# Kernel tuning notes

Hardware: AMD Instinct MI355X
Metric: run time of the kernel (lower is better)

## Reference

```python
import jax, jax.numpy as jnp
import numpy as np

NEG_SLOPE_GAT = 0.2   # PyG GATConv default negative_slope
NEG_SLOPE = 0.01      # torch.nn.LeakyReLU default
NUM_AISLES = 20       # aisle_nrs drawn from [0,20); matches aisle_nrs.max()+1


def leaky(x, s):
    return jnp.where(x >= 0, x, s * x)


def gat_conv(x, src, dst, W, a_src, a_dst, b, n_nodes):
    """Single-head PyG GATConv (self-loops already appended to src/dst)."""
    h = x @ W                                        # [N, C]
    es = h @ a_src                                   # [N]
    ed = h @ a_dst                                   # [N]
    e = leaky(es[src] + ed[dst], NEG_SLOPE_GAT)      # [E] per-edge score
    m = jax.ops.segment_max(e, dst, num_segments=n_nodes)
    w = jnp.exp(e - m[dst])
    z = jax.ops.segment_sum(w, dst, num_segments=n_nodes)
    alpha = w / z[dst]                               # segment softmax over incoming edges
    out = jax.ops.segment_sum(h[src] * alpha[:, None], dst, num_segments=n_nodes)
    return out + b


def setup_inputs() -> dict:
    key = jax.random.key(0)
    ks = jax.random.split(key, 32)
    B, N, E = 16, 2048, 32768
    Fin, H, O, HA = 32, 128, 64, 256

    def glorot(k, shape):
        fan = shape[0] + shape[-1]
        return jax.random.uniform(k, shape, jnp.float32, -1.0, 1.0) * np.sqrt(6.0 / fan)

    inp = {
        "graph_nodes": jax.random.normal(ks[0], (B, N, Fin), jnp.float32),
        "aisle_nrs": jax.random.randint(ks[1], (B, N), 0, NUM_AISLES),
        "graph_edge_links": jax.random.randint(ks[2], (B, 2, E), 0, N),
        "mask": jax.random.randint(ks[3], (B, N), 0, 2),
        "picks_left": jax.random.randint(ks[4], (B,), 0, 100),
        # GAT layer 1: Fin -> H
        "W1": glorot(ks[5], (Fin, H)), "as1": glorot(ks[6], (H,)), "ad1": glorot(ks[7], (H,)), "b1": jnp.zeros((H,), jnp.float32),
        # GAT layer 2: H -> H
        "W2": glorot(ks[8], (H, H)), "as2": glorot(ks[9], (H,)), "ad2": glorot(ks[10], (H,)), "b2": jnp.zeros((H,), jnp.float32),
        # GAT layer 3: H -> O
        "W3": glorot(ks[11], (H, O)), "as3": glorot(ks[12], (O,)), "ad3": glorot(ks[13], (O,)), "b3": jnp.zeros((O,), jnp.float32),
        # post-embedding MLP head
        "lw1": glorot(ks[14], (2 * O, HA)), "lb1": jnp.zeros((HA,), jnp.float32),
        "lw2": glorot(ks[15], (HA, O)), "lb2": jnp.zeros((O,), jnp.float32),
        "lw3": glorot(ks[16], (O, 1)), "lb3": jnp.zeros((1,), jnp.float32),
    }
    return inp


def reference(graph_nodes, aisle_nrs, graph_edge_links, mask, picks_left,
              W1, as1, ad1, b1, W2, as2, ad2, b2, W3, as3, ad3, b3,
              lw1, lb1, lw2, lb2, lw3, lb3):
    B, N, Fin = graph_nodes.shape
    NT = B * N
    x = graph_nodes.reshape(NT, Fin)

    # batch the graphs: offset per-graph edge indices, append self-loops
    off = (jnp.arange(B) * N)[:, None]
    src = (graph_edge_links[:, 0, :] + off).reshape(-1)
    dst = (graph_edge_links[:, 1, :] + off).reshape(-1)
    loops = jnp.arange(NT)
    src = jnp.concatenate([src, loops])
    dst = jnp.concatenate([dst, loops])

    x = gat_conv(x, src, dst, W1, as1, ad1, b1, NT)
    x = gat_conv(x, src, dst, W2, as2, ad2, b2, NT)
    x = gat_conv(x, src, dst, W3, as3, ad3, b3, NT)

    # scatter-mean aisle embedding
    batch_idx = jnp.repeat(jnp.arange(B), N)
    aid = aisle_nrs.reshape(-1) + batch_idx * NUM_AISLES   # [NT]
    S = B * NUM_AISLES
    ssum = jax.ops.segment_sum(x, aid, num_segments=S)
    cnt = jax.ops.segment_sum(jnp.ones((NT,), x.dtype), aid, num_segments=S)
    emb = ssum / jnp.maximum(cnt, 1.0)[:, None]

    x = jnp.concatenate([x, emb[aid]], axis=1)             # [NT, 2*O]
    x = leaky(x @ lw1 + lb1, NEG_SLOPE)
    x = leaky(x @ lw2 + lb2, NEG_SLOPE)
    x = (x @ lw3 + lb3).reshape(B, N)

    logits = jnp.where(mask != 0, x, -jnp.inf)
    return jax.nn.softmax(logits, axis=1)
```

## Files before the change

kernel.cpp:

```cpp
#include <hip/hip_runtime.h>
#include <hip/hip_bf16.h>
#include <math.h>
#include <stdint.h>

#define BATCH 16
#define NNODE 2048
#define EPG   32768
#define NT    (BATCH * NNODE)
#define ET    (BATCH * EPG + NT)
#define NUM_AISLES 20
#define SEG   (BATCH * NUM_AISLES)
#define NEG_GAT 0.2f
#define NEG_MLP 0.01f
#define ACHUNK 8
#define CAP 64
#define EMB_LD 72

typedef __attribute__((ext_vector_type(8))) short s16x8;
typedef __attribute__((ext_vector_type(4))) float f32x4;

__device__ __forceinline__ void split_bf16(float v, unsigned short& hi, unsigned short& lo) {
    unsigned int u = __float_as_uint(v);
    unsigned int r = u + 0x7FFFu + ((u >> 16) & 1u);
    hi = (unsigned short)(r >> 16);
    float fh = __uint_as_float(((unsigned int)hi) << 16);
    float rem = v - fh;
    unsigned int u2 = __float_as_uint(rem);
    unsigned int r2 = u2 + 0x7FFFu + ((u2 >> 16) & 1u);
    lo = (unsigned short)(r2 >> 16);
}

__device__ __forceinline__ unsigned int pack_bf16(float v) {
    unsigned short h, l;
    split_bf16(v, h, l);
    return ((unsigned int)h << 16) | l;
}

__device__ __forceinline__ float unpack_f32(unsigned int u) {
    return __uint_as_float(u & 0xffff0000u) + __uint_as_float(u << 16);
}

__device__ __forceinline__ int swz_row0(int bx) {
    int xcd = bx & 7, i = bx >> 3;
    int graph = xcd * 2 + (i >> 5);
    return graph * NNODE + (i & 31) * 64;
}

template <int K, int KC, int NOUT, int COLS>
__device__ __forceinline__ void prep_one(const float* __restrict__ W,
                                         unsigned short* __restrict__ dst, int idx) {
    constexpr int SWM = (KC >= 64) ? 7 : 3;
    int k = idx / NOUT, col = idx - k * NOUT;
    int ch = k / KC, kl = k - ch * KC;
    int ct = col / COLS, n = col - ct * COLS;
    int tile = ct * (K / KC) + ch;
    unsigned short h, l;
    split_bf16(W[idx], h, l);
    size_t base = (size_t)tile * (2 * COLS * KC);
    int pos = n * KC + (kl ^ ((n & SWM) << 3));
    dst[base + pos] = h;
    dst[base + COLS * KC + pos] = l;
}

__global__ __launch_bounds__(256) void prep_weights(const float* __restrict__ W1,
                                                    const float* __restrict__ W2,
                                                    const float* __restrict__ W3,
                                                    const float* __restrict__ lw1,
                                                    const float* __restrict__ lw2,
                                                    unsigned short* __restrict__ P1,
                                                    unsigned short* __restrict__ P2,
                                                    unsigned short* __restrict__ P3,
                                                    unsigned short* __restrict__ P4,
                                                    unsigned short* __restrict__ P5,
                                                    int* __restrict__ cnt) {
    int b = blockIdx.x, t = threadIdx.x;
    if (b < 16)        prep_one<32, 32, 128, 128>(W1, P1, b * 256 + t);
    else if (b < 80)   prep_one<128, 64, 128, 128>(W2, P2, (b - 16) * 256 + t);
    else if (b < 112)  prep_one<128, 128, 64, 64>(W3, P3, (b - 80) * 256 + t);
    else if (b < 240)  prep_one<128, 64, 256, 128>(lw1, P4, (b - 112) * 256 + t);
    else if (b < 304)  prep_one<256, 128, 64, 64>(lw2, P5, (b - 240) * 256 + t);
    else               cnt[(b - 304) * 256 + t] = 0;
}

__device__ __forceinline__ void scatter_body(int b, const int* __restrict__ links,
                                             int* __restrict__ cnt,
                                             int* __restrict__ col_bkt) {
    int s, d;
    if (b < 2048) {
        int xcd = b & 7, idx = b >> 3;
        int g = xcd * 2 + (idx >> 7);
        int chunk = idx & 127;
        int i = chunk * 256 + threadIdx.x;
        const int* pb = links + (size_t)g * 2 * EPG;
        s = pb[i] + (g << 11);
        d = pb[EPG + i] + (g << 11);
    } else {
        int b2 = b - 2048;
        int xcd = b2 & 7, idx = b2 >> 3;
        int g = xcd * 2 + (idx >> 3);
        int chunk = idx & 7;
        s = d = g * NNODE + chunk * 256 + threadIdx.x;
    }
    int pos = atomicAdd(&cnt[d], 1);
    if (pos < CAP) col_bkt[d * CAP + pos] = s;
}

template <int K, int KC, int NOUT, int COLS, bool LEAKY, bool ATTN, bool FINAL,
          bool CONCAT, bool PACKEDA, bool PACKOUT>
__device__ __forceinline__ void gemm_body(int bx, int by,
                                          const void* __restrict__ Aptr,
                                          const unsigned short* __restrict__ WP,
                                          const float* __restrict__ bias,
                                          void* __restrict__ outp,
                                          const float* __restrict__ a_src,
                                          const float* __restrict__ a_dst,
                                          float* __restrict__ es,
                                          float* __restrict__ ed,
                                          const float* __restrict__ psum,
                                          const int* __restrict__ pcnt,
                                          const int* __restrict__ aisle,
                                          const float* __restrict__ lw3,
                                          const float* __restrict__ lb3,
                                          const int* __restrict__ mask,
                                          float* __restrict__ logits) {
    constexpr int C = COLS / 16;
    constexpr int SWM = (KC >= 64) ? 7 : 3;
    constexpr int TILE_US = COLS * KC;
    constexpr int TB2 = 2 * TILE_US * 2;
    static_assert(TB2 % 4096 == 0, "chunk must be a multiple of one 256-thread 16B sweep");

    __shared__ unsigned short WS[2 * TILE_US];
    __shared__ float emb_s[CONCAT ? NUM_AISLES * EMB_LD : 1];

    const int tid = threadIdx.x;
    const int wave = tid >> 6, lane = tid & 63;
    const int quad = lane >> 4, l15 = lane & 15;
    const int row0 = swz_row0(bx);
    const int m = row0 + wave * 16 + l15;

    int am = 0;
    if constexpr (CONCAT) {
        int g = row0 >> 11;
        for (int i = tid; i < NUM_AISLES * 64; i += 256) {
            int a = i >> 6, f = i & 63;
            float s = 0.f;
            int c = 0;
#pragma unroll
            for (int ch = 0; ch < ACHUNK; ++ch) {
                s += psum[((size_t)(g * ACHUNK + ch) * NUM_AISLES + a) * 64 + f];
                c += pcnt[(g * ACHUNK + ch) * NUM_AISLES + a];
            }
            emb_s[a * EMB_LD + f] = s / fmaxf((float)c, 1.0f);
        }
        am = aisle[m];
    }

    f32x4 acc[C];
#pragma unroll
    for (int c = 0; c < C; ++c)
#pragma unroll
        for (int v = 0; v < 4; ++v) acc[c][v] = 0.f;

    union SU { s16x8 v; unsigned short u[8]; };

    for (int kb = 0; kb < K; kb += KC) {
        const char* gsrc = (const char*)WP
            + (size_t)(by * (K / KC) + kb / KC) * TB2;
#pragma unroll
        for (int s = 0; s < TB2 / 4096; ++s) {
            __builtin_amdgcn_global_load_lds(
                (const __attribute__((address_space(1))) void*)(gsrc + s * 4096 + wave * 1024 + lane * 16),
                (__attribute__((address_space(3))) void*)&WS[(s * 4096 + wave * 1024) >> 1],
                16, 0, 0);
        }
        __syncthreads();

        for (int kc = kb; kc < kb + KC; kc += 32) {
            const int off = kc + quad * 8;
            SU ah, al;
            if constexpr (CONCAT) {
                if (off < 64) {
                    const unsigned int* ap = (const unsigned int*)Aptr + (size_t)m * 64 + off;
                    uint4 u0 = ((const uint4*)ap)[0];
                    uint4 u1 = ((const uint4*)ap)[1];
                    unsigned int uu[8] = {u0.x, u0.y, u0.z, u0.w, u1.x, u1.y, u1.z, u1.w};
#pragma unroll
                    for (int j = 0; j < 8; ++j) {
                        ah.u[j] = (unsigned short)(uu[j] >> 16);
                        al.u[j] = (unsigned short)uu[j];
                    }
                } else {
                    const float* ep = &emb_s[am * EMB_LD + (off - 64)];
                    float4 v0 = ((const float4*)ep)[0];
                    float4 v1 = ((const float4*)ep)[1];
                    float a8[8] = {v0.x, v0.y, v0.z, v0.w, v1.x, v1.y, v1.z, v1.w};
#pragma unroll
                    for (int j = 0; j < 8; ++j) split_bf16(a8[j], ah.u[j], al.u[j]);
                }
            } else if constexpr (PACKEDA) {
                const unsigned int* ap = (const unsigned int*)Aptr + (size_t)m * K + off;
                uint4 u0 = ((const uint4*)ap)[0];
                uint4 u1 = ((const uint4*)ap)[1];
                unsigned int uu[8] = {u0.x, u0.y, u0.z, u0.w, u1.x, u1.y, u1.z, u1.w};
#pragma unroll
                for (int j = 0; j < 8; ++j) {
                    ah.u[j] = (unsigned short)(uu[j] >> 16);
                    al.u[j] = (unsigned short)uu[j];
                }
            } else {
                const float* srcp = (const float*)Aptr + (size_t)m * K + off;
                float4 v0 = ((const float4*)srcp)[0];
                float4 v1 = ((const float4*)srcp)[1];
                float a8[8] = {v0.x, v0.y, v0.z, v0.w, v1.x, v1.y, v1.z, v1.w};
#pragma unroll
                for (int j = 0; j < 8; ++j) split_bf16(a8[j], ah.u[j], al.u[j]);
            }

            const int kq = (kc - kb) + quad * 8;
#pragma unroll
            for (int c = 0; c < C; ++c) {
                int n = c * 16 + l15;
                int pos = n * KC + (kq ^ ((n & SWM) << 3));
                s16x8 wh = *(const s16x8*)&WS[pos];
                s16x8 wl = *(const s16x8*)&WS[TILE_US + pos];
                acc[c] = __builtin_amdgcn_mfma_f32_16x16x32_bf16(ah.v, wh, acc[c], 0, 0, 0);
                acc[c] = __builtin_amdgcn_mfma_f32_16x16x32_bf16(ah.v, wl, acc[c], 0, 0, 0);
                acc[c] = __builtin_amdgcn_mfma_f32_16x16x32_bf16(al.v, wh, acc[c], 0, 0, 0);
            }
        }
        if (kb + KC < K) __syncthreads();
    }
    if constexpr (FINAL) {
#pragma unroll
        for (int reg = 0; reg < 4; ++reg) {
            float p = 0.f;
#pragma unroll
            for (int c = 0; c < C; ++c) {
                int colx = c * 16 + l15;
                float v = acc[c][reg] + bias[colx];
                v = v >= 0.f ? v : NEG_MLP * v;
                p += v * lw3[colx];
            }
#pragma unroll
            for (int mk = 1; mk < 16; mk <<= 1) p += __shfl_xor(p, mk, 64);
            if (l15 == 0) {
                int row = row0 + wave * 16 + quad * 4 + reg;
                float lg = p + lb3[0];
                logits[row] = (mask[row] != 0) ? lg : -INFINITY;
            }
        }
    } else {
#pragma unroll
        for (int c = 0; c < C; ++c) {
            int colx = by * COLS + c * 16 + l15;
            float bv = bias ? bias[colx] : 0.f;
#pragma unroll
            for (int reg = 0; reg < 4; ++reg) {
                int row = row0 + wave * 16 + quad * 4 + reg;
                float v = acc[c][reg] + bv;
                if (LEAKY) v = v >= 0.f ? v : NEG_MLP * v;
                if constexpr (PACKOUT) {
                    ((unsigned int*)outp)[(size_t)row * NOUT + colx] = pack_bf16(v);
                } else {
                    ((float*)outp)[(size_t)row * NOUT + colx] = v;
                }
            }
        }
        if constexpr (ATTN) {
#pragma unroll
            for (int reg = 0; reg < 4; ++reg) {
                float ps = 0.f, pd = 0.f;
#pragma unroll
                for (int c = 0; c < C; ++c) {
                    int colx = c * 16 + l15;
                    float v = acc[c][reg];
                    ps += v * a_src[colx];
                    pd += v * a_dst[colx];
                }
#pragma unroll
                for (int mk = 1; mk < 16; mk <<= 1) {
                    ps += __shfl_xor(ps, mk, 64);
                    pd += __shfl_xor(pd, mk, 64);
                }
                if (l15 == 0) {
                    int row = row0 + wave * 16 + quad * 4 + reg;
                    es[row] = ps;
                    ed[row] = pd;
                }
            }
        }
    }
}

template <int K, int KC, int NOUT, int COLS, bool LEAKY, bool ATTN, bool FINAL,
          bool CONCAT, bool PACKEDA, bool PACKOUT>
__global__ __launch_bounds__(256) void gemm_mfma(const void* __restrict__ A,
                                                 const unsigned short* __restrict__ WP,
                                                 const float* __restrict__ bias,
                                                 void* __restrict__ out,
                                                 const float* __restrict__ a_src,
                                                 const float* __restrict__ a_dst,
                                                 float* __restrict__ es,
                                                 float* __restrict__ ed,
                                                 const float* __restrict__ psum,
                                                 const int* __restrict__ pcnt,
                                                 const int* __restrict__ aisle,
                                                 const float* __restrict__ lw3,
                                                 const float* __restrict__ lb3,
                                                 const int* __restrict__ mask,
                                                 float* __restrict__ logits) {
    gemm_body<K, KC, NOUT, COLS, LEAKY, ATTN, FINAL, CONCAT, PACKEDA, PACKOUT>(
        blockIdx.x, blockIdx.y, A, WP, bias, out, a_src, a_dst, es, ed,
        psum, pcnt, aisle, lw3, lb3, mask, logits);
}

__global__ __launch_bounds__(256) void gemm1_scatter(const float* __restrict__ A,
                                                     const unsigned short* __restrict__ WP,
                                                     float* __restrict__ out,
                                                     const float* __restrict__ a_src,
                                                     const float* __restrict__ a_dst,
                                                     float* __restrict__ es,
                                                     float* __restrict__ ed,
                                                     const int* __restrict__ links,
                                                     int* __restrict__ cnt,
                                                     int* __restrict__ col_bkt) {
    if (blockIdx.x >= NT / 64) {
        scatter_body(blockIdx.x - NT / 64, links, cnt, col_bkt);
        return;
    }
    gemm_body<32, 32, 128, 128, false, true, false, false, false, false>(
        blockIdx.x, 0, A, WP, nullptr, out, a_src, a_dst, es, ed,
        nullptr, nullptr, nullptr, nullptr, nullptr, nullptr, nullptr);
}

template <int HD>
__global__ __launch_bounds__(256) void gat_aggregate(const float* __restrict__ h,
                                                     const float* __restrict__ es,
                                                     const float* __restrict__ ed,
                                                     const int* __restrict__ cnt,
                                                     const int* __restrict__ col_bkt,
                                                     const float* __restrict__ bias,
                                                     unsigned int* __restrict__ out) {
    int b = blockIdx.x;
    int xcd = b & 7, q = b >> 3;
    int graph = xcd * 2 + (q >> 9);
    int node = graph * NNODE + (q & 511) * 4 + (threadIdx.x >> 6);
    int lane = threadIdx.x & 63;
    int deg = cnt[node];
    deg = deg < CAP ? deg : CAP;
    float edv = ed[node];

    float e0 = -INFINITY;
    int c0v = 0;
    if (lane < deg) {
        c0v = col_bkt[node * CAP + lane];
        float e = es[c0v] + edv;
        e0 = e >= 0.f ? e : NEG_GAT * e;
    }
    float m = e0;
#pragma unroll
    for (int off = 32; off; off >>= 1) m = fmaxf(m, __shfl_xor(m, off, 64));
    float z = __expf(e0 - m);
#pragma unroll
    for (int off = 32; off; off >>= 1) z += __shfl_xor(z, off, 64);
    float w0 = __expf(e0 - m) / z;

    const int quad = lane >> 4, l15 = lane & 15;
    if (HD == 128) {
        float a0 = 0.f, a1 = 0.f, a2 = 0.f, a3 = 0.f;
        float a4 = 0.f, a5 = 0.f, a6 = 0.f, a7 = 0.f;
        for (int jj = 0; jj < deg; jj += 4) {
            int j2 = jj + quad;
            int s = __shfl(c0v, j2, 64);
            float w = __shfl(w0, j2, 64);
            const float* base = h + (size_t)s * 128 + l15 * 8;
            float4 v0 = *(const float4*)base;
            float4 v1 = *(const float4*)(base + 4);
            a0 += w * v0.x; a1 += w * v0.y; a2 += w * v0.z; a3 += w * v0.w;
            a4 += w * v1.x; a5 += w * v1.y; a6 += w * v1.z; a7 += w * v1.w;
        }
#pragma unroll
        for (int off = 16; off <= 32; off <<= 1) {
            a0 += __shfl_xor(a0, off, 64); a1 += __shfl_xor(a1, off, 64);
            a2 += __shfl_xor(a2, off, 64); a3 += __shfl_xor(a3, off, 64);
            a4 += __shfl_xor(a4, off, 64); a5 += __shfl_xor(a5, off, 64);
            a6 += __shfl_xor(a6, off, 64); a7 += __shfl_xor(a7, off, 64);
        }
        if (quad == 0) {
            const float* bb = bias + l15 * 8;
            uint4 p0, p1;
            p0.x = pack_bf16(a0 + bb[0]); p0.y = pack_bf16(a1 + bb[1]);
            p0.z = pack_bf16(a2 + bb[2]); p0.w = pack_bf16(a3 + bb[3]);
            p1.x = pack_bf16(a4 + bb[4]); p1.y = pack_bf16(a5 + bb[5]);
            p1.z = pack_bf16(a6 + bb[6]); p1.w = pack_bf16(a7 + bb[7]);
            unsigned int* op = out + (size_t)node * 128 + l15 * 8;
            *(uint4*)op = p0;
            *(uint4*)(op + 4) = p1;
        }
    } else {
        float a0 = 0.f, a1 = 0.f, a2 = 0.f, a3 = 0.f;
        for (int jj = 0; jj < deg; jj += 4) {
            int j2 = jj + quad;
            int s = __shfl(c0v, j2, 64);
            float w = __shfl(w0, j2, 64);
            float4 v = *(const float4*)(h + (size_t)s * 64 + l15 * 4);
            a0 += w * v.x; a1 += w * v.y; a2 += w * v.z; a3 += w * v.w;
        }
#pragma unroll
        for (int off = 16; off <= 32; off <<= 1) {
            a0 += __shfl_xor(a0, off, 64); a1 += __shfl_xor(a1, off, 64);
            a2 += __shfl_xor(a2, off, 64); a3 += __shfl_xor(a3, off, 64);
        }
        if (quad == 0) {
            const float* bb = bias + l15 * 4;
            uint4 p;
            p.x = pack_bf16(a0 + bb[0]); p.y = pack_bf16(a1 + bb[1]);
            p.z = pack_bf16(a2 + bb[2]); p.w = pack_bf16(a3 + bb[3]);
            *(uint4*)(out + (size_t)node * 64 + l15 * 4) = p;
        }
    }
}

__global__ __launch_bounds__(256) void aisle_partial(const unsigned int* __restrict__ x3,
                                                     const int* __restrict__ aisle,
                                                     float* __restrict__ psum,
                                                     int* __restrict__ pcnt) {
    int xcd = blockIdx.x & 7, idx = blockIdx.x >> 3;
    int g = xcd * 2 + (idx >> 3);
    int ch = idx & 7;
    int pb = g * ACHUNK + ch;
    int f = threadIdx.x & 63;
    int stripe = threadIdx.x >> 6;

    __shared__ float sacc[4][NUM_AISLES][64];
    __shared__ int scnt[4][NUM_AISLES];
    for (int i = threadIdx.x; i < 4 * NUM_AISLES * 64; i += 256)
        ((float*)sacc)[i] = 0.f;
    for (int i = threadIdx.x; i < 4 * NUM_AISLES; i += 256)
        ((int*)scnt)[i] = 0;
    __syncthreads();

    const int* ai = aisle + g * NNODE;
    const unsigned int* xg = x3 + (size_t)g * NNODE * 64;
    int n0 = ch * 256 + stripe * 64;
#pragma unroll 4
    for (int i = 0; i < 64; ++i) {
        int n = n0 + i;
        int a = ai[n];
        float v = unpack_f32(xg[(size_t)n * 64 + f]);
        sacc[stripe][a][f] += v;
        if (f == 0) scnt[stripe][a]++;
    }
    __syncthreads();

    for (int i = threadIdx.x; i < NUM_AISLES * 64; i += 256) {
        int a = i >> 6, ff = i & 63;
        psum[((size_t)pb * NUM_AISLES + a) * 64 + ff] =
            sacc[0][a][ff] + sacc[1][a][ff] + sacc[2][a][ff] + sacc[3][a][ff];
    }
    for (int i = threadIdx.x; i < NUM_AISLES; i += 256) {
        pcnt[pb * NUM_AISLES + i] =
            scnt[0][i] + scnt[1][i] + scnt[2][i] + scnt[3][i];
    }
}

__global__ __launch_bounds__(256) void softmax_kernel(const float* __restrict__ logits,
                                                      float* __restrict__ out) {
    int b = blockIdx.x;
    const float* lr = logits + b * NNODE;
    __shared__ float red[4], redz[4];
    float m = -INFINITY;
    for (int i = threadIdx.x; i < NNODE; i += 256) m = fmaxf(m, lr[i]);
#pragma unroll
    for (int off = 32; off; off >>= 1) m = fmaxf(m, __shfl_xor(m, off, 64));
    if ((threadIdx.x & 63) == 0) red[threadIdx.x >> 6] = m;
    __syncthreads();
    m = fmaxf(fmaxf(red[0], red[1]), fmaxf(red[2], red[3]));
    float z = 0.f;
    for (int i = threadIdx.x; i < NNODE; i += 256) z += __expf(lr[i] - m);
#pragma unroll
    for (int off = 32; off; off >>= 1) z += __shfl_xor(z, off, 64);
    if ((threadIdx.x & 63) == 0) redz[threadIdx.x >> 6] = z;
    __syncthreads();
    z = redz[0] + redz[1] + redz[2] + redz[3];
    float invz = 1.0f / z;
    for (int i = threadIdx.x; i < NNODE; i += 256) {
        float v = lr[i];
        out[b * NNODE + i] = (v == -INFINITY) ? 0.f : __expf(v - m) * invz;
    }
}


extern "C" void kernel_launch(void* const* d_in, const int* in_sizes, int n_in,
                              void* d_out, int out_size, void* d_ws, size_t ws_size,
                              hipStream_t stream) {
    const float* gn   = (const float*)d_in[0];
    const int* aisle  = (const int*)d_in[1];
    const int* links  = (const int*)d_in[2];
    const int* mask   = (const int*)d_in[3];
    const float* W1  = (const float*)d_in[5];
    const float* as1 = (const float*)d_in[6];
    const float* ad1 = (const float*)d_in[7];
    const float* b1  = (const float*)d_in[8];
    const float* W2  = (const float*)d_in[9];
    const float* as2 = (const float*)d_in[10];
    const float* ad2 = (const float*)d_in[11];
    const float* b2  = (const float*)d_in[12];
    const float* W3  = (const float*)d_in[13];
    const float* as3 = (const float*)d_in[14];
    const float* ad3 = (const float*)d_in[15];
    const float* b3  = (const float*)d_in[16];
    const float* lw1 = (const float*)d_in[17];
    const float* lb1 = (const float*)d_in[18];
    const float* lw2 = (const float*)d_in[19];
    const float* lb2 = (const float*)d_in[20];
    const float* lw3 = (const float*)d_in[21];
    const float* lb3 = (const float*)d_in[22];
    float* out = (float*)d_out;

    float* ws = (float*)d_ws;
    float* h      = ws;
    float* xb     = h + (size_t)NT * 128;
    float* es     = xb + (size_t)NT * 128;
    float* ed     = es + NT;
    float* emb    = ed + NT;
    float* y1     = emb + SEG * 64;
    float* y2     = y1 + (size_t)NT * 256;
    float* logits = y2 + (size_t)NT * 64;
    float* psum   = logits + NT;
    int* pcnt     = (int*)(psum + 128 * NUM_AISLES * 64);
    int* row_ptr  = pcnt + 128 * NUM_AISLES;
    int* cnt      = row_ptr + NT + 1;
    int* col_bkt  = (int*)y2;

    unsigned short* wsplit = (unsigned short*)(((uintptr_t)(cnt + NT) + 255) & ~(uintptr_t)255);
    unsigned short* P1 = wsplit;
    unsigned short* P2 = P1 + 8192;
    unsigned short* P3 = P2 + 32768;
    unsigned short* P4 = P3 + 16384;
    unsigned short* P5 = P4 + 65536;

    const int EB = (ET + 255) / 256;

    prep_weights<<<432, 256, 0, stream>>>(W1, W2, W3, lw1, lw2, P1, P2, P3, P4, P5, cnt);

    gemm1_scatter<<<NT / 64 + EB, 256, 0, stream>>>(gn, P1, h, as1, ad1, es, ed,
                                                    links, cnt, col_bkt);
    gat_aggregate<128><<<NT / 4, 256, 0, stream>>>(h, es, ed, cnt, col_bkt, b1, (unsigned int*)xb);

    gemm_mfma<128, 64, 128, 128, false, true, false, false, true, false><<<dim3(NT / 64, 1), 256, 0, stream>>>(
        xb, P2, nullptr, h, as2, ad2, es, ed, nullptr, nullptr, nullptr, nullptr, nullptr, nullptr, nullptr);
    gat_aggregate<128><<<NT / 4, 256, 0, stream>>>(h, es, ed, cnt, col_bkt, b2, (unsigned int*)xb);

    gemm_mfma<128, 128, 64, 64, false, true, false, false, true, false><<<dim3(NT / 64, 1), 256, 0, stream>>>(
        xb, P3, nullptr, h, as3, ad3, es, ed, nullptr, nullptr, nullptr, nullptr, nullptr, nullptr, nullptr);
    gat_aggregate<64><<<NT / 4, 256, 0, stream>>>(h, es, ed, cnt, col_bkt, b3, (unsigned int*)xb);

    aisle_partial<<<BATCH * ACHUNK, 256, 0, stream>>>((const unsigned int*)xb, aisle, psum, pcnt);

    gemm_mfma<128, 64, 256, 128, true, false, false, true, false, true><<<dim3(NT / 64, 2), 256, 0, stream>>>(
        xb, P4, lb1, y1, nullptr, nullptr, nullptr, nullptr, psum, pcnt, aisle, nullptr, nullptr, nullptr, nullptr);

    gemm_mfma<256, 128, 64, 64, true, false, true, false, true, false><<<dim3(NT / 64, 1), 256, 0, stream>>>(
        y1, P5, lb2, nullptr, nullptr, nullptr, nullptr, nullptr, nullptr, nullptr, nullptr, lw3, lb3, mask, logits);

    softmax_kernel<<<BATCH, 256, 0, stream>>>(logits, out);
}
```

Measured before the change: 279.1 us.

## Fuse all stages into one cooperative persistent kernel with grid syncs

Replaces the sequence of about ten kernel launches (weight prep, GEMM plus edge scatter, three aggregations, aisle partials, MLP GEMMs, softmax) with one cooperative persistent kernel. Each stage loops over virtual block indices and a grid-wide sync separates stages. Static shared buffers become a single shared arena that the stage bodies carve up. This aims to remove launch gaps and tail effects between stages. The cost is grid-sync overhead, a grid capped at 1024 blocks, the loss of the per-stage XCD-aware block mapping in some stages, and occupancy limited by the union of the stages' register and shared-memory needs.

Result: slower. 935.9 us (+235.3%).

```diff
diff --git a/kernel.cpp b/kernel.cpp
--- a/kernel.cpp
+++ b/kernel.cpp
@@ -1,7 +1,10 @@
 #include <hip/hip_runtime.h>
+#include <hip/hip_cooperative_groups.h>
 #include <hip/hip_bf16.h>
 #include <math.h>
 #include <stdint.h>
+
+namespace cg = cooperative_groups;
 
 #define BATCH 16
 #define NNODE 2048
@@ -15,6 +18,7 @@
 #define ACHUNK 8
 #define CAP 64
 #define EMB_LD 72
+#define SMEM_BYTES 38528
 
 typedef __attribute__((ext_vector_type(8))) short s16x8;
 typedef __attribute__((ext_vector_type(4))) float f32x4;
@@ -62,18 +66,19 @@
     dst[base + COLS * KC + pos] = l;
 }
 
-__global__ __launch_bounds__(256) void prep_weights(const float* __restrict__ W1,
-                                                    const float* __restrict__ W2,
-                                                    const float* __restrict__ W3,
-                                                    const float* __restrict__ lw1,
-                                                    const float* __restrict__ lw2,
-                                                    unsigned short* __restrict__ P1,
-                                                    unsigned short* __restrict__ P2,
-                                                    unsigned short* __restrict__ P3,
-                                                    unsigned short* __restrict__ P4,
-                                                    unsigned short* __restrict__ P5,
-                                                    int* __restrict__ cnt) {
-    int b = blockIdx.x, t = threadIdx.x;
+__device__ __forceinline__ void prep_body(int b,
+                                          const float* __restrict__ W1,
+                                          const float* __restrict__ W2,
+                                          const float* __restrict__ W3,
+                                          const float* __restrict__ lw1,
+                                          const float* __restrict__ lw2,
+                                          unsigned short* __restrict__ P1,
+                                          unsigned short* __restrict__ P2,
+                                          unsigned short* __restrict__ P3,
+                                          unsigned short* __restrict__ P4,
+                                          unsigned short* __restrict__ P5,
+                                          int* __restrict__ cnt) {
+    int t = threadIdx.x;
     if (b < 16)        prep_one<32, 32, 128, 128>(W1, P1, b * 256 + t);
     else if (b < 80)   prep_one<128, 64, 128, 128>(W2, P2, (b - 16) * 256 + t);
     else if (b < 112)  prep_one<128, 128, 64, 64>(W3, P3, (b - 80) * 256 + t);
@@ -107,7 +112,7 @@
 
 template <int K, int KC, int NOUT, int COLS, bool LEAKY, bool ATTN, bool FINAL,
           bool CONCAT, bool PACKEDA, bool PACKOUT>
-__device__ __forceinline__ void gemm_body(int bx, int by,
+__device__ __forceinline__ void gemm_body(int bx, int by, unsigned char* smem,
                                           const void* __restrict__ Aptr,
                                           const unsigned short* __restrict__ WP,
                                           const float* __restrict__ bias,
@@ -128,9 +133,12 @@
     constexpr int TILE_US = COLS * KC;
     constexpr int TB2 = 2 * TILE_US * 2;
     static_assert(TB2 % 4096 == 0, "chunk must be a multiple of one 256-thread 16B sweep");
-
-    __shared__ unsigned short WS[2 * TILE_US];
-    __shared__ float emb_s[CONCAT ? NUM_AISLES * EMB_LD : 1];
+    static_assert(TB2 <= 32768, "W-stage arena overflow");
+
+    unsigned short* WS = (unsigned short*)smem;
+    float* emb_s = (float*)(smem + 32768);
+
+    __syncthreads();
 
     const int tid = threadIdx.x;
     const int wave = tid >> 6, lane = tid & 63;
@@ -292,56 +300,15 @@
     }
 }
 
-template <int K, int KC, int NOUT, int COLS, bool LEAKY, bool ATTN, bool FINAL,
-          bool CONCAT, bool PACKEDA, bool PACKOUT>
-__global__ __launch_bounds__(256) void gemm_mfma(const void* __restrict__ A,
-                                                 const unsigned short* __restrict__ WP,
-                                                 const float* __restrict__ bias,
-                                                 void* __restrict__ out,
-                                                 const float* __restrict__ a_src,
-                                                 const float* __restrict__ a_dst,
-                                                 float* __restrict__ es,
-                                                 float* __restrict__ ed,
-                                                 const float* __restrict__ psum,
-                                                 const int* __restrict__ pcnt,
-                                                 const int* __restrict__ aisle,
-                                                 const float* __restrict__ lw3,
-                                                 const float* __restrict__ lb3,
-                                                 const int* __restrict__ mask,
-                                                 float* __restrict__ logits) {
-    gemm_body<K, KC, NOUT, COLS, LEAKY, ATTN, FINAL, CONCAT, PACKEDA, PACKOUT>(
-        blockIdx.x, blockIdx.y, A, WP, bias, out, a_src, a_dst, es, ed,
-        psum, pcnt, aisle, lw3, lb3, mask, logits);
-}
-
-__global__ __launch_bounds__(256) void gemm1_scatter(const float* __restrict__ A,
-                                                     const unsigned short* __restrict__ WP,
-                                                     float* __restrict__ out,
-                                                     const float* __restrict__ a_src,
-                                                     const float* __restrict__ a_dst,
-                                                     float* __restrict__ es,
-                                                     float* __restrict__ ed,
-                                                     const int* __restrict__ links,
-                                                     int* __restrict__ cnt,
-                                                     int* __restrict__ col_bkt) {
-    if (blockIdx.x >= NT / 64) {
-        scatter_body(blockIdx.x - NT / 64, links, cnt, col_bkt);
-        return;
-    }
-    gemm_body<32, 32, 128, 128, false, true, false, false, false, false>(
-        blockIdx.x, 0, A, WP, nullptr, out, a_src, a_dst, es, ed,
-        nullptr, nullptr, nullptr, nullptr, nullptr, nullptr, nullptr);
-}
-
 template <int HD>
-__global__ __launch_bounds__(256) void gat_aggregate(const float* __restrict__ h,
-                                                     const float* __restrict__ es,
-                                                     const float* __restrict__ ed,
-                                                     const int* __restrict__ cnt,
-                                                     const int* __restrict__ col_bkt,
-                                                     const float* __restrict__ bias,
-                                                     unsigned int* __restrict__ out) {
-    int b = blockIdx.x;
+__device__ __forceinline__ void agg_body(int b,
+                                         const float* __restrict__ h,
+                                         const float* __restrict__ es,
+                                         const float* __restrict__ ed,
+                                         const int* __restrict__ cnt,
+                                         const int* __restrict__ col_bkt,
+                                         const float* __restrict__ bias,
+                                         unsigned int* __restrict__ out) {
     int xcd = b & 7, q = b >> 3;
     int graph = xcd * 2 + (q >> 9);
     int node = graph * NNODE + (q & 511) * 4 + (threadIdx.x >> 6);
@@ -421,23 +388,22 @@
     }
 }
 
-__global__ __launch_bounds__(256) void aisle_partial(const unsigned int* __restrict__ x3,
-                                                     const int* __restrict__ aisle,
-                                                     float* __restrict__ psum,
-                                                     int* __restrict__ pcnt) {
-    int xcd = blockIdx.x & 7, idx = blockIdx.x >> 3;
-    int g = xcd * 2 + (idx >> 3);
-    int ch = idx & 7;
-    int pb = g * ACHUNK + ch;
+__device__ __forceinline__ void partial_body(int b, unsigned char* smem,
+                                             const unsigned int* __restrict__ x3,
+                                             const int* __restrict__ aisle,
+                                             float* __restrict__ psum,
+                                             int* __restrict__ pcnt) {
+    int g = b >> 3;
+    int ch = b & 7;
     int f = threadIdx.x & 63;
     int stripe = threadIdx.x >> 6;
 
-    __shared__ float sacc[4][NUM_AISLES][64];
-    __shared__ int scnt[4][NUM_AISLES];
-    for (int i = threadIdx.x; i < 4 * NUM_AISLES * 64; i += 256)
-        ((float*)sacc)[i] = 0.f;
-    for (int i = threadIdx.x; i < 4 * NUM_AISLES; i += 256)
-        ((int*)scnt)[i] = 0;
+    float* sacc = (float*)smem;
+    int* scnt = (int*)(smem + 20480);
+
+    __syncthreads();
+    for (int i = threadIdx.x; i < 4 * NUM_AISLES * 64; i += 256) sacc[i] = 0.f;
+    for (int i = threadIdx.x; i < 4 * NUM_AISLES; i += 256) scnt[i] = 0;
     __syncthreads();
 
     const int* ai = aisle + g * NNODE;
@@ -448,27 +414,31 @@
         int n = n0 + i;
         int a = ai[n];
         float v = unpack_f32(xg[(size_t)n * 64 + f]);
-        sacc[stripe][a][f] += v;
-        if (f == 0) scnt[stripe][a]++;
+        sacc[(stripe * NUM_AISLES + a) * 64 + f] += v;
+        if (f == 0) scnt[stripe * NUM_AISLES + a]++;
     }
     __syncthreads();
 
     for (int i = threadIdx.x; i < NUM_AISLES * 64; i += 256) {
         int a = i >> 6, ff = i & 63;
-        psum[((size_t)pb * NUM_AISLES + a) * 64 + ff] =
-            sacc[0][a][ff] + sacc[1][a][ff] + sacc[2][a][ff] + sacc[3][a][ff];
+        psum[((size_t)b * NUM_AISLES + a) * 64 + ff] =
+            sacc[(0 * NUM_AISLES + a) * 64 + ff] + sacc[(1 * NUM_AISLES + a) * 64 + ff] +
+            sacc[(2 * NUM_AISLES + a) * 64 + ff] + sacc[(3 * NUM_AISLES + a) * 64 + ff];
     }
     for (int i = threadIdx.x; i < NUM_AISLES; i += 256) {
-        pcnt[pb * NUM_AISLES + i] =
-            scnt[0][i] + scnt[1][i] + scnt[2][i] + scnt[3][i];
-    }
-}
-
-__global__ __launch_bounds__(256) void softmax_kernel(const float* __restrict__ logits,
-                                                      float* __restrict__ out) {
-    int b = blockIdx.x;
+        pcnt[b * NUM_AISLES + i] =
+            scnt[0 * NUM_AISLES + i] + scnt[1 * NUM_AISLES + i] +
+            scnt[2 * NUM_AISLES + i] + scnt[3 * NUM_AISLES + i];
+    }
+}
+
+__device__ __forceinline__ void softmax_body(int b, unsigned char* smem,
+                                             const float* __restrict__ logits,
+                                             float* __restrict__ out) {
     const float* lr = logits + b * NNODE;
-    __shared__ float red[4], redz[4];
+    float* red = (float*)smem;
+    float* redz = red + 4;
+    __syncthreads();
     float m = -INFINITY;
     for (int i = threadIdx.x; i < NNODE; i += 256) m = fmaxf(m, lr[i]);
 #pragma unroll
@@ -488,6 +458,94 @@
         float v = lr[i];
         out[b * NNODE + i] = (v == -INFINITY) ? 0.f : __expf(v - m) * invz;
     }
+}
+
+__global__ __launch_bounds__(256, 4) void mega(
+    const float* __restrict__ gn, const int* __restrict__ aisle,
+    const int* __restrict__ links, const int* __restrict__ mask,
+    const float* __restrict__ W1, const float* __restrict__ as1,
+    const float* __restrict__ ad1, const float* __restrict__ b1,
+    const float* __restrict__ W2, const float* __restrict__ as2,
+    const float* __restrict__ ad2, const float* __restrict__ b2,
+    const float* __restrict__ W3, const float* __restrict__ as3,
+    const float* __restrict__ ad3, const float* __restrict__ b3,
+    const float* __restrict__ lw1, const float* __restrict__ lb1,
+    const float* __restrict__ lw2, const float* __restrict__ lb2,
+    const float* __restrict__ lw3, const float* __restrict__ lb3,
+    float* __restrict__ h, unsigned int* __restrict__ xb,
+    float* __restrict__ es, float* __restrict__ ed,
+    unsigned int* __restrict__ y1, float* __restrict__ logits,
+    float* __restrict__ psum, int* __restrict__ pcnt,
+    int* __restrict__ cnt, int* __restrict__ col_bkt,
+    unsigned short* __restrict__ P1, unsigned short* __restrict__ P2,
+    unsigned short* __restrict__ P3, unsigned short* __restrict__ P4,
+    unsigned short* __restrict__ P5, float* __restrict__ out) {
+    cg::grid_group grid = cg::this_grid();
+    const int b0 = blockIdx.x;
+    const int nb = gridDim.x;
+    __shared__ alignas(16) unsigned char smem[SMEM_BYTES];
+
+    for (int vb = b0; vb < 432; vb += nb)
+        prep_body(vb, W1, W2, W3, lw1, lw2, P1, P2, P3, P4, P5, cnt);
+    grid.sync();
+
+    for (int vb = b0; vb < 2688; vb += nb) {
+        if (vb < 512)
+            gemm_body<32, 32, 128, 128, false, true, false, false, false, false>(
+                vb, 0, smem, gn, P1, nullptr, (void*)h, as1, ad1, es, ed,
+                nullptr, nullptr, nullptr, nullptr, nullptr, nullptr, nullptr);
+        else
+            scatter_body(vb - 512, links, cnt, col_bkt);
+    }
+    grid.sync();
+
+    for (int vb = b0; vb < 8192; vb += nb)
+        agg_body<128>(vb, h, es, ed, cnt, col_bkt, b1, xb);
+    grid.sync();
+
+    for (int vb = b0; vb < 1024; vb += nb)
+        if ((vb & 1) == 0)
+            gemm_body<128, 64, 128, 128, false, true, false, false, true, false>(
+                vb >> 1, 0, smem, xb, P2, nullptr, (void*)h, as2, ad2, es, ed,
+                nullptr, nullptr, nullptr, nullptr, nullptr, nullptr, nullptr);
+    grid.sync();
+
+    for (int vb = b0; vb < 8192; vb += nb)
+        agg_body<128>(vb, h, es, ed, cnt, col_bkt, b2, xb);
+    grid.sync();
+
+    for (int vb = b0; vb < 1024; vb += nb)
+        if ((vb & 1) == 0)
+            gemm_body<128, 128, 64, 64, false, true, false, false, true, false>(
+                vb >> 1, 0, smem, xb, P3, nullptr, (void*)h, as3, ad3, es, ed,
+                nullptr, nullptr, nullptr, nullptr, nullptr, nullptr, nullptr);
+    grid.sync();
+
+    for (int vb = b0; vb < 8192; vb += nb)
+        agg_body<64>(vb, h, es, ed, cnt, col_bkt, b3, xb);
+    grid.sync();
+
+    for (int vb = b0; vb < 1024; vb += nb)
+        if ((vb & 7) == 0)
+            partial_body(vb >> 3, smem, xb, aisle, psum, pcnt);
+    grid.sync();
+
+    for (int vb = b0; vb < 1024; vb += nb)
+        gemm_body<128, 64, 256, 128, true, false, false, true, false, true>(
+            vb & 511, vb >> 9, smem, xb, P4, lb1, (void*)y1, nullptr, nullptr,
+            nullptr, nullptr, psum, pcnt, aisle, nullptr, nullptr, nullptr, nullptr);
+    grid.sync();
+
+    for (int vb = b0; vb < 1024; vb += nb)
+        if ((vb & 1) == 0)
+            gemm_body<256, 128, 64, 64, true, false, true, false, true, false>(
+                vb >> 1, 0, smem, y1, P5, lb2, nullptr, nullptr, nullptr,
+                nullptr, nullptr, nullptr, nullptr, nullptr, lw3, lb3, mask, logits);
+    grid.sync();
+
+    for (int vb = b0; vb < 1024; vb += nb)
+        if ((vb & 63) == 0)
+            softmax_body(vb >> 6, smem, logits, out);
 }
 
 
@@ -540,29 +598,27 @@
     unsigned short* P4 = P3 + 16384;
     unsigned short* P5 = P4 + 65536;
 
-    const int EB = (ET + 255) / 256;
-
-    prep_weights<<<432, 256, 0, stream>>>(W1, W2, W3, lw1, lw2, P1, P2, P3, P4, P5, cnt);
-
-    gemm1_scatter<<<NT / 64 + EB, 256, 0, stream>>>(gn, P1, h, as1, ad1, es, ed,
-                                                    links, cnt, col_bkt);
-    gat_aggregate<128><<<NT / 4, 256, 0, stream>>>(h, es, ed, cnt, col_bkt, b1, (unsigned int*)xb);
-
-    gemm_mfma<128, 64, 128, 128, false, true, false, false, true, false><<<dim3(NT / 64, 1), 256, 0, stream>>>(
-        xb, P2, nullptr, h, as2, ad2, es, ed, nullptr, nullptr, nullptr, nullptr, nullptr, nullptr, nullptr);
-    gat_aggregate<128><<<NT / 4, 256, 0, stream>>>(h, es, ed, cnt, col_bkt, b2, (unsigned int*)xb);
-
-    gemm_mfma<128, 128, 64, 64, false, true, false, false, true, false><<<dim3(NT / 64, 1), 256, 0, stream>>>(
-        xb, P3, nullptr, h, as3, ad3, es, ed, nullptr, nullptr, nullptr, nullptr, nullptr, nullptr, nullptr);
-    gat_aggregate<64><<<NT / 4, 256, 0, stream>>>(h, es, ed, cnt, col_bkt, b3, (unsigned int*)xb);
-
-    aisle_partial<<<BATCH * ACHUNK, 256, 0, stream>>>((const unsigned int*)xb, aisle, psum, pcnt);
-
-    gemm_mfma<128, 64, 256, 128, true, false, false, true, false, true><<<dim3(NT / 64, 2), 256, 0, stream>>>(
-        xb, P4, lb1, y1, nullptr, nullptr, nullptr, nullptr, psum, pcnt, aisle, nullptr, nullptr, nullptr, nullptr);
-
-    gemm_mfma<256, 128, 64, 64, true, false, true, false, true, false><<<dim3(NT / 64, 1), 256, 0, stream>>>(
-        y1, P5, lb2, nullptr, nullptr, nullptr, nullptr, nullptr, nullptr, nullptr, nullptr, lw3, lb3, mask, logits);
-
-    softmax_kernel<<<BATCH, 256, 0, stream>>>(logits, out);
-}
+    unsigned int* xbp = (unsigned int*)xb;
+    unsigned int* y1p = (unsigned int*)y1;
+
+    int maxb = 0;
+    hipOccupancyMaxActiveBlocksPerMultiprocessor(&maxb, mega, 256, 0);
+    int gridsz = maxb * 256;
+    if (gridsz > 1024) gridsz = 1024;
+    if (gridsz < 8) gridsz = 8;
+
+    void* kargs[] = {
+        (void*)&gn, (void*)&aisle, (void*)&links, (void*)&mask,
+        (void*)&W1, (void*)&as1, (void*)&ad1, (void*)&b1,
+        (void*)&W2, (void*)&as2, (void*)&ad2, (void*)&b2,
+        (void*)&W3, (void*)&as3, (void*)&ad3, (void*)&b3,
+        (void*)&lw1, (void*)&lb1, (void*)&lw2, (void*)&lb2,
+        (void*)&lw3, (void*)&lb3,
+        (void*)&h, (void*)&xbp, (void*)&es, (void*)&ed,
+        (void*)&y1p, (void*)&logits, (void*)&psum, (void*)&pcnt,
+        (void*)&cnt, (void*)&col_bkt,
+        (void*)&P1, (void*)&P2, (void*)&P3, (void*)&P4, (void*)&P5,
+        (void*)&out };
+
+    hipLaunchCooperativeKernel(mega, dim3(gridsz), dim3(256), kargs, 0, stream);
+}
```

## Halve GEMM row tile to 32 and split output columns across wave pairs

Applied to the files above, without the earlier changes.

Each GEMM block now covers 32 rows instead of 64. Its four waves form a 2x2 grid: two row groups of 16, each paired with one half of the output columns. This doubles the grid size and halves the accumulator registers per wave, aiming for more parallelism and occupancy. The cost is that every block loads the same weight tile for half as many rows. The attention-score and final-logit row reductions now combine partial sums across wave pairs through shared memory and an extra barrier.

After: 292.9 us. +5.0%, slower.

```diff
diff --git a/kernel.cpp b/kernel.cpp
--- a/kernel.cpp
+++ b/kernel.cpp
@@ -42,8 +42,8 @@
 
 __device__ __forceinline__ int swz_row0(int bx) {
     int xcd = bx & 7, i = bx >> 3;
-    int graph = xcd * 2 + (i >> 5);
-    return graph * NNODE + (i & 31) * 64;
+    int graph = xcd * 2 + (i >> 6);
+    return graph * NNODE + (i & 63) * 32;
 }
 
 template <int K, int KC, int NOUT, int COLS>
@@ -123,7 +123,7 @@
                                           const float* __restrict__ lb3,
                                           const int* __restrict__ mask,
                                           float* __restrict__ logits) {
-    constexpr int C = COLS / 16;
+    constexpr int C = COLS / 32;
     constexpr int SWM = (KC >= 64) ? 7 : 3;
     constexpr int TILE_US = COLS * KC;
     constexpr int TB2 = 2 * TILE_US * 2;
@@ -131,12 +131,16 @@
 
     __shared__ unsigned short WS[2 * TILE_US];
     __shared__ float emb_s[CONCAT ? NUM_AISLES * EMB_LD : 1];
+    __shared__ float2 comb[(ATTN || FINAL) ? 32 : 1];
 
     const int tid = threadIdx.x;
     const int wave = tid >> 6, lane = tid & 63;
     const int quad = lane >> 4, l15 = lane & 15;
+    const int rw = wave & 1;
+    const int ch = wave >> 1;
+    const int cb = ch * (COLS / 2);
     const int row0 = swz_row0(bx);
-    const int m = row0 + wave * 16 + l15;
+    const int m = row0 + rw * 16 + l15;
 
     int am = 0;
     if constexpr (CONCAT) {
@@ -146,9 +150,9 @@
             float s = 0.f;
             int c = 0;
 #pragma unroll
-            for (int ch = 0; ch < ACHUNK; ++ch) {
-                s += psum[((size_t)(g * ACHUNK + ch) * NUM_AISLES + a) * 64 + f];
-                c += pcnt[(g * ACHUNK + ch) * NUM_AISLES + a];
+            for (int chh = 0; chh < ACHUNK; ++chh) {
+                s += psum[((size_t)(g * ACHUNK + chh) * NUM_AISLES + a) * 64 + f];
+                c += pcnt[(g * ACHUNK + chh) * NUM_AISLES + a];
             }
             emb_s[a * EMB_LD + f] = s / fmaxf((float)c, 1.0f);
         }
@@ -219,7 +223,7 @@
             const int kq = (kc - kb) + quad * 8;
 #pragma unroll
             for (int c = 0; c < C; ++c) {
-                int n = c * 16 + l15;
+                int n = cb + c * 16 + l15;
                 int pos = n * KC + (kq ^ ((n & SWM) << 3));
                 s16x8 wh = *(const s16x8*)&WS[pos];
                 s16x8 wl = *(const s16x8*)&WS[TILE_US + pos];
@@ -231,32 +235,44 @@
         if (kb + KC < K) __syncthreads();
     }
     if constexpr (FINAL) {
+        float pr[4];
 #pragma unroll
         for (int reg = 0; reg < 4; ++reg) {
             float p = 0.f;
 #pragma unroll
             for (int c = 0; c < C; ++c) {
-                int colx = c * 16 + l15;
+                int colx = cb + c * 16 + l15;
                 float v = acc[c][reg] + bias[colx];
                 v = v >= 0.f ? v : NEG_MLP * v;
                 p += v * lw3[colx];
             }
 #pragma unroll
             for (int mk = 1; mk < 16; mk <<= 1) p += __shfl_xor(p, mk, 64);
-            if (l15 == 0) {
-                int row = row0 + wave * 16 + quad * 4 + reg;
-                float lg = p + lb3[0];
+            pr[reg] = p;
+        }
+        if (ch == 1 && l15 == 0) {
+#pragma unroll
+            for (int reg = 0; reg < 4; ++reg)
+                comb[rw * 16 + quad * 4 + reg].x = pr[reg];
+        }
+        __syncthreads();
+        if (ch == 0 && l15 == 0) {
+#pragma unroll
+            for (int reg = 0; reg < 4; ++reg) {
+                int lr = rw * 16 + quad * 4 + reg;
+                int row = row0 + lr;
+                float lg = pr[reg] + comb[lr].x + lb3[0];
                 logits[row] = (mask[row] != 0) ? lg : -INFINITY;
             }
         }
     } else {
 #pragma unroll
         for (int c = 0; c < C; ++c) {
-            int colx = by * COLS + c * 16 + l15;
+            int colx = by * COLS + cb + c * 16 + l15;
             float bv = bias ? bias[colx] : 0.f;
 #pragma unroll
             for (int reg = 0; reg < 4; ++reg) {
-                int row = row0 + wave * 16 + quad * 4 + reg;
+                int row = row0 + rw * 16 + quad * 4 + reg;
                 float v = acc[c][reg] + bv;
                 if (LEAKY) v = v >= 0.f ? v : NEG_MLP * v;
                 if constexpr (PACKOUT) {
@@ -267,12 +283,13 @@
             }
         }
         if constexpr (ATTN) {
+            float psr[4], pdr[4];
 #pragma unroll
             for (int reg = 0; reg < 4; ++reg) {
                 float ps = 0.f, pd = 0.f;
 #pragma unroll
                 for (int c = 0; c < C; ++c) {
-                    int colx = c * 16 + l15;
+                    int colx = cb + c * 16 + l15;
                     float v = acc[c][reg];
                     ps += v * a_src[colx];
                     pd += v * a_dst[colx];
@@ -282,10 +299,24 @@
                     ps += __shfl_xor(ps, mk, 64);
                     pd += __shfl_xor(pd, mk, 64);
                 }
-                if (l15 == 0) {
-                    int row = row0 + wave * 16 + quad * 4 + reg;
-                    es[row] = ps;
-                    ed[row] = pd;
+                psr[reg] = ps;
+                pdr[reg] = pd;
+            }
+            if (ch == 1 && l15 == 0) {
+#pragma unroll
+                for (int reg = 0; reg < 4; ++reg) {
+                    comb[rw * 16 + quad * 4 + reg].x = psr[reg];
+                    comb[rw * 16 + quad * 4 + reg].y = pdr[reg];
+                }
+            }
+            __syncthreads();
+            if (ch == 0 && l15 == 0) {
+#pragma unroll
+                for (int reg = 0; reg < 4; ++reg) {
+                    int lr = rw * 16 + quad * 4 + reg;
+                    int row = row0 + lr;
+                    es[row] = psr[reg] + comb[lr].x;
+                    ed[row] = pdr[reg] + comb[lr].y;
                 }
             }
         }
@@ -324,8 +355,8 @@
                                                      const int* __restrict__ links,
                                                      int* __restrict__ cnt,
                                                      int* __restrict__ col_bkt) {
-    if (blockIdx.x >= NT / 64) {
-        scatter_body(blockIdx.x - NT / 64, links, cnt, col_bkt);
+    if (blockIdx.x >= NT / 32) {
+        scatter_body(blockIdx.x - NT / 32, links, cnt, col_bkt);
         return;
     }
     gemm_body<32, 32, 128, 128, false, true, false, false, false, false>(
@@ -544,24 +575,24 @@
 
     prep_weights<<<432, 256, 0, stream>>>(W1, W2, W3, lw1, lw2, P1, P2, P3, P4, P5, cnt);
 
-    gemm1_scatter<<<NT / 64 + EB, 256, 0, stream>>>(gn, P1, h, as1, ad1, es, ed,
+    gemm1_scatter<<<NT / 32 + EB, 256, 0, stream>>>(gn, P1, h, as1, ad1, es, ed,
                                                     links, cnt, col_bkt);
     gat_aggregate<128><<<NT / 4, 256, 0, stream>>>(h, es, ed, cnt, col_bkt, b1, (unsigned int*)xb);
 
-    gemm_mfma<128, 64, 128, 128, false, true, false, false, true, false><<<dim3(NT / 64, 1), 256, 0, stream>>>(
+    gemm_mfma<128, 64, 128, 128, false, true, false, false, true, false><<<dim3(NT / 32, 1), 256, 0, stream>>>(
         xb, P2, nullptr, h, as2, ad2, es, ed, nullptr, nullptr, nullptr, nullptr, nullptr, nullptr, nullptr);
     gat_aggregate<128><<<NT / 4, 256, 0, stream>>>(h, es, ed, cnt, col_bkt, b2, (unsigned int*)xb);
 
-    gemm_mfma<128, 128, 64, 64, false, true, false, false, true, false><<<dim3(NT / 64, 1), 256, 0, stream>>>(
+    gemm_mfma<128, 128, 64, 64, false, true, false, false, true, false><<<dim3(NT / 32, 1), 256, 0, stream>>>(
         xb, P3, nullptr, h, as3, ad3, es, ed, nullptr, nullptr, nullptr, nullptr, nullptr, nullptr, nullptr);
     gat_aggregate<64><<<NT / 4, 256, 0, stream>>>(h, es, ed, cnt, col_bkt, b3, (unsigned int*)xb);
 
     aisle_partial<<<BATCH * ACHUNK, 256, 0, stream>>>((const unsigned int*)xb, aisle, psum, pcnt);
 
-    gemm_mfma<128, 64, 256, 128, true, false, false, true, false, true><<<dim3(NT / 64, 2), 256, 0, stream>>>(
+    gemm_mfma<128, 64, 256, 128, true, false, false, true, false, true><<<dim3(NT / 32, 2), 256, 0, stream>>>(
         xb, P4, lb1, y1, nullptr, nullptr, nullptr, nullptr, psum, pcnt, aisle, nullptr, nullptr, nullptr, nullptr);
 
-    gemm_mfma<256, 128, 64, 64, true, false, true, false, true, false><<<dim3(NT / 64, 1), 256, 0, stream>>>(
+    gemm_mfma<256, 128, 64, 64, true, false, true, false, true, false><<<dim3(NT / 32, 1), 256, 0, stream>>>(
         y1, P5, lb2, nullptr, nullptr, nullptr, nullptr, nullptr, nullptr, nullptr, nullptr, lw3, lb3, mask, logits);
 
     softmax_kernel<<<BATCH, 256, 0, stream>>>(logits, out);
```
